# Kernel tuning notes

Hardware: AMD Instinct MI355X
Metric: run time of the kernel (lower is better)

## Reference

```python
import jax, jax.numpy as jnp
import numpy as np

EMB_DIM = 64
NUM_USERS = 1_000_000
NUM_ITEMS = 1_000_000
NUM_GROUPS = 100_000
NUM_MEMBERS = 3_200_000
BATCH = 16_384


def setup_inputs() -> dict:
    key = jax.random.key(0)
    ks = jax.random.split(key, 10)
    # xavier-uniform-ish embedding tables
    bound_u = float(np.sqrt(6.0 / (NUM_USERS + EMB_DIM)))
    bound_i = float(np.sqrt(6.0 / (NUM_ITEMS + EMB_DIM)))
    user_emb = jax.random.uniform(ks[0], (NUM_USERS, EMB_DIM), jnp.float32, -bound_u, bound_u)
    item_emb = jax.random.uniform(ks[1], (NUM_ITEMS, EMB_DIM), jnp.float32, -bound_i, bound_i)
    # PredictLayer: Linear(emb_dim, 8) -> ReLU -> Linear(8, 1)
    w1 = jax.random.normal(ks[2], (EMB_DIM, 8), jnp.float32) * (1.0 / np.sqrt(EMB_DIM))
    b1 = jnp.zeros((8,), jnp.float32)
    w2 = jax.random.normal(ks[3], (8, 1), jnp.float32) * (1.0 / np.sqrt(8))
    b2 = jnp.zeros((1,), jnp.float32)
    # flattened ragged group_number_dict: member i of group member_groups[i] is user member_users[i]
    member_users = jax.random.randint(ks[4], (NUM_MEMBERS,), 0, NUM_USERS)
    member_groups = jnp.sort(jax.random.randint(ks[5], (NUM_MEMBERS,), 0, NUM_GROUPS))
    group_inputs = jax.random.randint(ks[6], (BATCH,), 0, NUM_GROUPS)
    item_inputs = jax.random.randint(ks[7], (BATCH,), 0, NUM_ITEMS)
    return {
        "user_emb": user_emb, "item_emb": item_emb,
        "w1": w1, "b1": b1, "w2": w2, "b2": b2,
        "member_users": member_users, "member_groups": member_groups,
        "group_inputs": group_inputs, "item_inputs": item_inputs,
        "num_groups": NUM_GROUPS,
    }


def reference(user_emb, item_emb, w1, b1, w2, b2,
              member_users, member_groups, group_inputs, item_inputs, num_groups):
    # segment-mean of user embeddings per group (replaces the per-group python loop)
    member_emb = user_emb[member_users]                       # [M, D] gather
    sums = jax.ops.segment_sum(member_emb, member_groups,
                               num_segments=num_groups, indices_are_sorted=True)   # [G, D]
    counts = jax.ops.segment_sum(jnp.ones(member_users.shape, user_emb.dtype), member_groups,
                                 num_segments=num_groups, indices_are_sorted=True)  # [G]
    group_mean = sums / jnp.maximum(counts, 1.0)[:, None]     # [G, D]
    g_emb = group_mean[group_inputs]                          # [B, D]
    i_emb = item_emb[item_inputs]                             # [B, D]
    x = g_emb * i_emb                                         # [B, D]
    h = jax.nn.relu(x @ w1 + b1)                              # [B, 8]
    return jax.nn.sigmoid(h @ w2 + b2)                        # [B, 1]
```

## Files before the change

### kernel.cpp

```cpp
#include <hip/hip_runtime.h>
#include <math.h>

#define EMB 64

__global__ __launch_bounds__(256) void boundaries_kernel(
    const int* __restrict__ member_groups,
    int num_members,
    const int* __restrict__ num_groups_p,
    int* __restrict__ offs)
{
    const int j = blockIdx.x * blockDim.x + threadIdx.x;
    if (j >= num_members) return;
    const int gj = member_groups[j];
    if (j == 0) {
        for (int g = 0; g <= gj; ++g) offs[g] = 0;
    } else {
        const int gp = member_groups[j - 1];
        for (int g = gp + 1; g <= gj; ++g) offs[g] = j;
    }
    if (j == num_members - 1) {
        const int G = *num_groups_p;
        for (int g = gj + 1; g <= G; ++g) offs[g] = num_members;
    }
}

__global__ __launch_bounds__(256) void consrec_kernel(
    const float* __restrict__ user_emb,
    const float* __restrict__ item_emb,
    const float* __restrict__ w1,
    const float* __restrict__ b1,
    const float* __restrict__ w2,
    const float* __restrict__ b2,
    const int*   __restrict__ member_users,
    const int*   __restrict__ offs,
    const int*   __restrict__ group_inputs,
    const int*   __restrict__ item_inputs,
    int batch,
    float* __restrict__ out)
{
    const int wave = (int)((blockIdx.x * blockDim.x + threadIdx.x) >> 6);
    const int lane = threadIdx.x & 63;
    if (wave >= batch) return;

    const int g     = group_inputs[wave];
    const int start = offs[g];
    const int end   = offs[g + 1];
    const int cnt   = end - start;

    float sum = 0.f;
    for (int base = start; base < end; base += 64) {
        const int m = min(64, end - base);
        const int uvec = (lane < m) ? member_users[base + lane] : 0;
        int j = 0;
        for (; j + 4 <= m; j += 4) {
            const int u0 = __builtin_amdgcn_readlane(uvec, j + 0);
            const int u1 = __builtin_amdgcn_readlane(uvec, j + 1);
            const int u2 = __builtin_amdgcn_readlane(uvec, j + 2);
            const int u3 = __builtin_amdgcn_readlane(uvec, j + 3);
            const float a0 = user_emb[((size_t)u0 << 6) + lane];
            const float a1 = user_emb[((size_t)u1 << 6) + lane];
            const float a2 = user_emb[((size_t)u2 << 6) + lane];
            const float a3 = user_emb[((size_t)u3 << 6) + lane];
            sum += a0; sum += a1; sum += a2; sum += a3;
        }
        for (; j < m; ++j) {
            const int u = __builtin_amdgcn_readlane(uvec, j);
            sum += user_emb[((size_t)u << 6) + lane];
        }
    }
    const float mean = sum / (float)(cnt > 0 ? cnt : 1);

    const float x = mean * item_emb[(size_t)item_inputs[wave] * EMB + lane];

    float p[8];
    #pragma unroll
    for (int k = 0; k < 8; ++k) p[k] = x * w1[lane * 8 + k];

    #pragma unroll
    for (int off = 32; off >= 1; off >>= 1) {
        #pragma unroll
        for (int k = 0; k < 8; ++k) p[k] += __shfl_xor(p[k], off, 64);
    }

    float acc = b2[0];
    #pragma unroll
    for (int k = 0; k < 8; ++k) {
        float h = p[k] + b1[k];
        h = h > 0.f ? h : 0.f;
        acc += h * w2[k];
    }
    const float y = 1.f / (1.f + expf(-acc));
    if (lane == 0) out[wave] = y;
}

extern "C" void kernel_launch(void* const* d_in, const int* in_sizes, int n_in,
                              void* d_out, int out_size, void* d_ws, size_t ws_size,
                              hipStream_t stream) {
    const float* user_emb      = (const float*)d_in[0];
    const float* item_emb      = (const float*)d_in[1];
    const float* w1            = (const float*)d_in[2];
    const float* b1            = (const float*)d_in[3];
    const float* w2            = (const float*)d_in[4];
    const float* b2            = (const float*)d_in[5];
    const int*   member_users  = (const int*)d_in[6];
    const int*   member_groups = (const int*)d_in[7];
    const int*   group_inputs  = (const int*)d_in[8];
    const int*   item_inputs   = (const int*)d_in[9];
    const int*   num_groups_p  = (const int*)d_in[10];

    const int num_members = in_sizes[6];
    const int batch       = in_sizes[8];

    int* offs = (int*)d_ws;

    {
        const int threads = 256;
        const int grid = (num_members + threads - 1) / threads;
        boundaries_kernel<<<grid, threads, 0, stream>>>(
            member_groups, num_members, num_groups_p, offs);
    }
    {
        const int threads = 256;
        const int waves_per_block = threads / 64;
        const int grid = (batch + waves_per_block - 1) / waves_per_block;
        consrec_kernel<<<grid, threads, 0, stream>>>(
            user_emb, item_emb, w1, b1, w2, b2,
            member_users, offs, group_inputs, item_inputs,
            batch, (float*)d_out);
    }
}
```

Measured before the change: 443.4 us.

## Gather member embeddings as float4 with four rows per wave instruction

The wave is split into four 16-lane subgroups, and each subgroup loads a whole 64-float user row as float4 vectors. Each load instruction therefore fetches four member rows instead of one, with 16 rows in flight per unrolled iteration. Partial sums are merged across subgroups with xor shuffles, and the item multiply and first linear layer are rewritten around the 4-wide layout with a shorter reduction. The aim is fewer memory instructions and more outstanding row fetches, at the cost of extra shuffles and index broadcasts through __shfl rather than readlane.

```diff
diff --git a/kernel.cpp b/kernel.cpp
--- a/kernel.cpp
+++ b/kernel.cpp
@@ -2,6 +2,8 @@
 #include <math.h>
 
 #define EMB 64
+
+typedef float f32x4 __attribute__((ext_vector_type(4)));
 
 __global__ __launch_bounds__(256) void boundaries_kernel(
     const int* __restrict__ member_groups,
@@ -42,42 +44,65 @@
     const int lane = threadIdx.x & 63;
     if (wave >= batch) return;
 
+    const int sub = lane >> 4;
+    const int q   = lane & 15;
+
     const int g     = group_inputs[wave];
     const int start = offs[g];
     const int end   = offs[g + 1];
     const int cnt   = end - start;
 
-    float sum = 0.f;
+    f32x4 s4 = {0.f, 0.f, 0.f, 0.f};
     for (int base = start; base < end; base += 64) {
         const int m = min(64, end - base);
         const int uvec = (lane < m) ? member_users[base + lane] : 0;
         int j = 0;
-        for (; j + 4 <= m; j += 4) {
-            const int u0 = __builtin_amdgcn_readlane(uvec, j + 0);
-            const int u1 = __builtin_amdgcn_readlane(uvec, j + 1);
-            const int u2 = __builtin_amdgcn_readlane(uvec, j + 2);
-            const int u3 = __builtin_amdgcn_readlane(uvec, j + 3);
-            const float a0 = user_emb[((size_t)u0 << 6) + lane];
-            const float a1 = user_emb[((size_t)u1 << 6) + lane];
-            const float a2 = user_emb[((size_t)u2 << 6) + lane];
-            const float a3 = user_emb[((size_t)u3 << 6) + lane];
-            sum += a0; sum += a1; sum += a2; sum += a3;
+        for (; j + 16 <= m; j += 16) {
+            const int u0 = __shfl(uvec, j + 0  + sub, 64);
+            const int u1 = __shfl(uvec, j + 4  + sub, 64);
+            const int u2 = __shfl(uvec, j + 8  + sub, 64);
+            const int u3 = __shfl(uvec, j + 12 + sub, 64);
+            const f32x4 v0 = *(const f32x4*)(user_emb + ((size_t)u0 << 6) + (q << 2));
+            const f32x4 v1 = *(const f32x4*)(user_emb + ((size_t)u1 << 6) + (q << 2));
+            const f32x4 v2 = *(const f32x4*)(user_emb + ((size_t)u2 << 6) + (q << 2));
+            const f32x4 v3 = *(const f32x4*)(user_emb + ((size_t)u3 << 6) + (q << 2));
+            s4 += v0; s4 += v1; s4 += v2; s4 += v3;
         }
-        for (; j < m; ++j) {
-            const int u = __builtin_amdgcn_readlane(uvec, j);
-            sum += user_emb[((size_t)u << 6) + lane];
+        for (; j < m; j += 4) {
+            const int mi = j + sub;
+            const int u  = __shfl(uvec, mi & 63, 64);
+            if (mi < m) {
+                const f32x4 v = *(const f32x4*)(user_emb + ((size_t)u << 6) + (q << 2));
+                s4 += v;
+            }
         }
     }
-    const float mean = sum / (float)(cnt > 0 ? cnt : 1);
 
-    const float x = mean * item_emb[(size_t)item_inputs[wave] * EMB + lane];
+    #pragma unroll
+    for (int off = 16; off <= 32; off <<= 1) {
+        f32x4 t;
+        t.x = __shfl_xor(s4.x, off, 64);
+        t.y = __shfl_xor(s4.y, off, 64);
+        t.z = __shfl_xor(s4.z, off, 64);
+        t.w = __shfl_xor(s4.w, off, 64);
+        s4 += t;
+    }
+
+    const float inv = 1.f / (float)(cnt > 0 ? cnt : 1);
+    const f32x4 item4 = *(const f32x4*)(item_emb + ((size_t)item_inputs[wave] << 6) + (q << 2));
+    const f32x4 x4 = s4 * inv * item4;
 
     float p[8];
     #pragma unroll
-    for (int k = 0; k < 8; ++k) p[k] = x * w1[lane * 8 + k];
-
+    for (int k = 0; k < 8; ++k) {
+        const int d0 = q << 2;
+        p[k] = x4.x * w1[(d0 + 0) * 8 + k]
+             + x4.y * w1[(d0 + 1) * 8 + k]
+             + x4.z * w1[(d0 + 2) * 8 + k]
+             + x4.w * w1[(d0 + 3) * 8 + k];
+    }
     #pragma unroll
-    for (int off = 32; off >= 1; off >>= 1) {
+    for (int off = 1; off <= 8; off <<= 1) {
         #pragma unroll
         for (int k = 0; k < 8; ++k) p[k] += __shfl_xor(p[k], off, 64);
     }
```

Result: no change. 447.2 us (+0.9%).
